# Performance work log

Hardware: AMD Instinct MI355X
Metric: run time of the kernel (lower is better)

## Reference

```python
import jax, jax.numpy as jnp
import numpy as np

B, L, D = 2, 2048, 1024
H = 16
DH = D // H
FACTOR = 0.6
U = max(1, min(L, int(FACTOR * L)))  # 1228 selected queries


def setup_inputs() -> dict:
    key = jax.random.key(0)
    ks = jax.random.split(key, 9)
    s = 0.02
    return {
        "x": jax.random.normal(ks[0], (B, L, D), dtype=jnp.float32),
        "Wq": jax.random.normal(ks[1], (D, D), dtype=jnp.float32) * s,
        "bq": jnp.zeros((D,), dtype=jnp.float32),
        "Wk": jax.random.normal(ks[2], (D, D), dtype=jnp.float32) * s,
        "bk": jnp.zeros((D,), dtype=jnp.float32),
        "Wv": jax.random.normal(ks[3], (D, D), dtype=jnp.float32) * s,
        "bv": jnp.zeros((D,), dtype=jnp.float32),
        "Wo": jax.random.normal(ks[4], (D, D), dtype=jnp.float32) * s,
        "bo": jnp.zeros((D,), dtype=jnp.float32),
    }


def _split_heads(x):
    b, l, d = x.shape
    return x.reshape(b, l, H, DH).transpose(0, 2, 1, 3)  # [b,h,l,dh]


def reference(x, Wq, bq, Wk, bk, Wv, bv, Wo, bo):
    b, l, _ = x.shape
    scale = 1.0 / jnp.sqrt(jnp.asarray(DH, dtype=x.dtype))

    q = _split_heads(x @ Wq + bq)  # [b,h,l,dh]
    k = _split_heads(x @ Wk + bk)
    v = _split_heads(x @ Wv + bv)

    # full scores for sparsity heuristic
    scores = jnp.einsum("bhqd,bhkd->bhqk", q, k) * scale  # [b,h,l,l]
    sparsity = scores.max(axis=-1) - scores.mean(axis=-1)  # [b,h,l]

    _, top_idx = jax.lax.top_k(sparsity, U)  # [b,h,U]

    # gather selected queries, attend only on those rows
    q_sel = jnp.take_along_axis(q, top_idx[..., None], axis=2)  # [b,h,U,dh]
    scores_sel = jnp.einsum("bhud,bhkd->bhuk", q_sel, k) * scale  # [b,h,U,l]
    attn = jax.nn.softmax(scores_sel, axis=-1)
    out_sel = jnp.einsum("bhuk,bhkd->bhud", attn, v)  # [b,h,U,dh]

    # scatter back into zero-initialized output
    bi = jnp.arange(b)[:, None, None]
    hi = jnp.arange(H)[None, :, None]
    out = jnp.zeros_like(q).at[bi, hi, top_idx].set(out_sel)  # [b,h,l,dh]

    out = out.transpose(0, 2, 1, 3).reshape(b, l, D)
    return out @ Wo + bo
```

## Files before the change

### kernel.cpp

```cpp
#include <hip/hip_runtime.h>
#include <math.h>
#include <stdint.h>

#define Bn 2
#define Ln 2048
#define Dn 1024
#define Hn 16
#define DHn 64
#define Un 1228
#define BHn (Bn*Hn)
#define SCALE 0.125f
#define WIN 32
#define WHALF 16
#define SXf 16.0f
#define SWf 256.0f
#define SQf 16.0f
#define SVf 16.0f
#define SPf 16.0f
#define ESC_PROJ (1.0f / 4096.0f)
#define ESC_OUT  (1.0f / 65536.0f)
#define PSC (SCALE / 256.0f)
#define QPS 88

typedef _Float16 f16;
typedef __attribute__((ext_vector_type(8))) _Float16 f16x8;
typedef __attribute__((ext_vector_type(4))) float f32x4;
struct h4s { f16 x, y, z, w; };

__device__ __forceinline__ void splitf16(float f, f16& hi, f16& lo) {
  hi = (f16)f;
  lo = (f16)(f - (float)hi);
}

__device__ __forceinline__ void gl_lds16(const void* g, void* l) {
  __builtin_amdgcn_global_load_lds(
      (const __attribute__((address_space(1))) void*)g,
      (__attribute__((address_space(3))) void*)l, 16, 0, 0);
}

#define MFMA(a, b, c) __builtin_amdgcn_mfma_f32_16x16x32_f16((a), (b), (c), 0, 0, 0)

__global__ __launch_bounds__(256) void split_kernel(
    const float* __restrict__ in, f16* __restrict__ oh, f16* __restrict__ ol, int n4) {
  int i = blockIdx.x * 256 + threadIdx.x;
  if (i >= n4) return;
  float4 v = ((const float4*)in)[i];
  h4s h, l;
  splitf16(v.x * SXf, h.x, l.x); splitf16(v.y * SXf, h.y, l.y);
  splitf16(v.z * SXf, h.z, l.z); splitf16(v.w * SXf, h.w, l.w);
  ((h4s*)oh)[i] = h; ((h4s*)ol)[i] = l;
}

__global__ __launch_bounds__(256) void tsplit_w4(
    const float* __restrict__ W0, const float* __restrict__ W1,
    const float* __restrict__ W2, const float* __restrict__ W3,
    f16* __restrict__ oh, f16* __restrict__ ol) {
  __shared__ float ts[64][65];
  const int t = threadIdx.x;
  const int r0 = blockIdx.x * 64, c0 = blockIdx.y * 64;
  const int z = blockIdx.z;
  const float* in = (z == 0) ? W0 : (z == 1) ? W1 : (z == 2) ? W2 : W3;
#pragma unroll
  for (int c = 0; c < 4; ++c) {
    int f = (c * 256 + t) * 4; int row = f >> 6, col = f & 63;
    float4 v = *(const float4*)&in[(size_t)(r0 + row) * Dn + c0 + col];
    ts[row][col] = v.x; ts[row][col + 1] = v.y; ts[row][col + 2] = v.z; ts[row][col + 3] = v.w;
  }
  __syncthreads();
#pragma unroll
  for (int c = 0; c < 4; ++c) {
    int f = (c * 256 + t) * 4; int crow = f >> 6, rcol = f & 63;
    h4s h, l;
    splitf16(ts[rcol + 0][crow] * SWf, h.x, l.x);
    splitf16(ts[rcol + 1][crow] * SWf, h.y, l.y);
    splitf16(ts[rcol + 2][crow] * SWf, h.z, l.z);
    splitf16(ts[rcol + 3][crow] * SWf, h.w, l.w);
    size_t o = (size_t)(z * 1024 + c0 + crow) * Dn + r0 + rcol;
    *(h4s*)&oh[o] = h; *(h4s*)&ol[o] = l;
  }
}

__global__ void gemm_qkv(
    const f16* __restrict__ Ah, const f16* __restrict__ Al,
    const f16* __restrict__ Bth, const f16* __restrict__ Btl,
    const float* __restrict__ bq, const float* __restrict__ bk, const float* __restrict__ bv,
    float* __restrict__ Qf, f16* __restrict__ Qbh,
    float* __restrict__ Kf, f16* __restrict__ Kbh,
    f16* __restrict__ Vh16, int K) {
  __shared__ f16 sAh[128 * 32], sAl[128 * 32], sBh[128 * 32], sBl[128 * 32];
  const int t = threadIdx.x;
  const int w = t >> 6, lane = t & 63, lm = lane & 15, q = lane >> 4;
  const int wr = w >> 1, wc = w & 1;
  const int n0 = blockIdx.x * 128, m0 = blockIdx.y * 128;
  f32x4 acc[4][4] = {};
  for (int k0 = 0; k0 < K; k0 += 32) {
    const f16* s0 = Ah + (size_t)m0 * K + k0;
    const f16* s1 = Al + (size_t)m0 * K + k0;
    const f16* s2 = Bth + (size_t)n0 * K + k0;
    const f16* s3 = Btl + (size_t)n0 * K + k0;
#pragma unroll
    for (int c = 0; c < 2; ++c) {
      int f = (c * 256 + t) * 8; int row = f >> 5, col = f & 31;
      size_t go = (size_t)row * K + col;
      gl_lds16(s0 + go, &sAh[f]);
      gl_lds16(s1 + go, &sAl[f]);
      gl_lds16(s2 + go, &sBh[f]);
      gl_lds16(s3 + go, &sBl[f]);
    }
    __syncthreads();
    f16x8 a_h[4], a_l[4], b_h[4], b_l[4];
#pragma unroll
    for (int mi = 0; mi < 4; ++mi) {
      int r = (wr * 64 + mi * 16 + lm) * 32 + q * 8;
      a_h[mi] = *(const f16x8*)&sAh[r];
      a_l[mi] = *(const f16x8*)&sAl[r];
    }
#pragma unroll
    for (int ni = 0; ni < 4; ++ni) {
      int r = (wc * 64 + ni * 16 + lm) * 32 + q * 8;
      b_h[ni] = *(const f16x8*)&sBh[r];
      b_l[ni] = *(const f16x8*)&sBl[r];
    }
#pragma unroll
    for (int mi = 0; mi < 4; ++mi)
#pragma unroll
      for (int ni = 0; ni < 4; ++ni) {
        acc[mi][ni] = MFMA(a_h[mi], b_h[ni], acc[mi][ni]);
        acc[mi][ni] = MFMA(a_h[mi], b_l[ni], acc[mi][ni]);
        acc[mi][ni] = MFMA(a_l[mi], b_h[ni], acc[mi][ni]);
      }
    __syncthreads();
  }
#pragma unroll
  for (int mi = 0; mi < 4; ++mi)
#pragma unroll
    for (int ni = 0; ni < 4; ++ni) {
      int nglob = n0 + wc * 64 + ni * 16;
      int seg = nglob >> 10;
      int c = (nglob & 1023) + lm;
      const float* bp = (seg == 0) ? bq : (seg == 1) ? bk : bv;
      float bvv = bp[c];
#pragma unroll
      for (int r = 0; r < 4; ++r) {
        int grow = m0 + wr * 64 + mi * 16 + q * 4 + r;
        float v = acc[mi][ni][r] * ESC_PROJ + bvv;
        size_t o = (size_t)grow * 1024 + c;
        if (seg == 0) {
          Qf[o] = v;
          Qbh[o] = (f16)(v * SQf);
        } else if (seg == 1) {
          Kf[o] = v;
          Kbh[o] = (f16)(v * SQf);
        } else {
          Vh16[o] = (f16)(v * SVf);
        }
      }
    }
}

__global__ __launch_bounds__(256) void tsplit_v(
    const f16* __restrict__ Vh16, f16* __restrict__ out) {
  __shared__ f16 ts[64][72];
  const int t = threadIdx.x;
  const int l0 = blockIdx.x * 64;
  const int bh = blockIdx.y, b = bh >> 4, h = bh & 15;
#pragma unroll
  for (int c = 0; c < 2; ++c) {
    int e = c * 256 + t; int row = e >> 3, cg = e & 7;
    *(uint4*)&ts[row][cg * 8] =
        *(const uint4*)&Vh16[((size_t)b * Ln + l0 + row) * Dn + h * DHn + cg * 8];
  }
  __syncthreads();
#pragma unroll
  for (int c = 0; c < 2; ++c) {
    int e = c * 256 + t; int drow = e >> 3, lg = e & 7;
    f16 tmp[8];
#pragma unroll
    for (int j = 0; j < 8; ++j) tmp[j] = ts[lg * 8 + j][drow];
    *(uint4*)&out[((size_t)bh * DHn + drow) * Ln + l0 + lg * 8] = *(uint4*)tmp;
  }
}

__global__ __launch_bounds__(256, 4) void gemm_a1(
    const f16* __restrict__ A,
    const f16* __restrict__ Bth, const f16* __restrict__ Btl,
    const float* __restrict__ bias, float escale,
    float* __restrict__ Cf, int M, int N, int K) {
  __shared__ f16 sA[128 * 32], sBh[64 * 32], sBl[64 * 32];
  const int t = threadIdx.x;
  const int w = t >> 6, lane = t & 63, lm = lane & 15, q = lane >> 4;
  const int wr = w >> 1, wc = w & 1;
  const int n0 = blockIdx.x * 64, m0 = blockIdx.y * 128;
  f32x4 acc[4][2] = {};
  for (int k0 = 0; k0 < K; k0 += 32) {
    const f16* s0 = A + (size_t)m0 * K + k0;
    const f16* s2 = Bth + (size_t)n0 * K + k0;
    const f16* s3 = Btl + (size_t)n0 * K + k0;
#pragma unroll
    for (int c = 0; c < 2; ++c) {
      int f = (c * 256 + t) * 8; int row = f >> 5, col = f & 31;
      gl_lds16(s0 + (size_t)row * K + col, &sA[f]);
    }
    {
      int f = t * 8; int row = f >> 5, col = f & 31;
      gl_lds16(s2 + (size_t)row * K + col, &sBh[f]);
      gl_lds16(s3 + (size_t)row * K + col, &sBl[f]);
    }
    __syncthreads();
    f16x8 a_[4], b_h[2], b_l[2];
#pragma unroll
    for (int mi = 0; mi < 4; ++mi)
      a_[mi] = *(const f16x8*)&sA[(wr * 64 + mi * 16 + lm) * 32 + q * 8];
#pragma unroll
    for (int ni = 0; ni < 2; ++ni) {
      int r = (wc * 32 + ni * 16 + lm) * 32 + q * 8;
      b_h[ni] = *(const f16x8*)&sBh[r];
      b_l[ni] = *(const f16x8*)&sBl[r];
    }
#pragma unroll
    for (int mi = 0; mi < 4; ++mi)
#pragma unroll
      for (int ni = 0; ni < 2; ++ni) {
        acc[mi][ni] = MFMA(a_[mi], b_h[ni], acc[mi][ni]);
        acc[mi][ni] = MFMA(a_[mi], b_l[ni], acc[mi][ni]);
      }
    __syncthreads();
  }
#pragma unroll
  for (int mi = 0; mi < 4; ++mi)
#pragma unroll
    for (int ni = 0; ni < 2; ++ni) {
      int gcol = n0 + wc * 32 + ni * 16 + lm;
      float bvv = bias[gcol];
#pragma unroll
      for (int r = 0; r < 4; ++r) {
        int grow = m0 + wr * 64 + mi * 16 + q * 4 + r;
        Cf[(size_t)grow * N + gcol] = acc[mi][ni][r] * escale + bvv;
      }
    }
}

__global__ __launch_bounds__(256) void ksum_part(
    const f16* __restrict__ Kh, float* __restrict__ ksum) {
  __shared__ float red[4][64];
  const int t = threadIdx.x, d = t & 63, seg = t >> 6;
  const int bx = blockIdx.x, bh = blockIdx.y, b = bh >> 4, h = bh & 15;
  float s = 0.f;
  const int lbase = bx * 256 + seg * 64;
  for (int r = 0; r < 64; ++r) {
    size_t o = ((size_t)b * Ln + lbase + r) * Dn + h * DHn + d;
    s += (float)Kh[o];
  }
  red[seg][d] = s;
  __syncthreads();
  if (t < 64) atomicAdd(&ksum[bh * DHn + t], red[0][t] + red[1][t] + red[2][t] + red[3][t]);
}

__global__ __launch_bounds__(256, 2) void attn_stats_mfma(
    const f16* __restrict__ Qh, const f16* __restrict__ Kh,
    const float* __restrict__ ksum,
    float* __restrict__ row_max, float* __restrict__ spars) {
  __shared__ f16 sQh[128 * 64], sKh[128 * 64];
  __shared__ float redm[128][5];
  const int t = threadIdx.x;
  const int w = t >> 6, lane = t & 63, lm = lane & 15, q = lane >> 4;
  const int bh = blockIdx.y, b = bh >> 4, h = bh & 15;
  const int q0 = blockIdx.x * 128;
  const f16* qsh = Qh + ((size_t)b * Ln + q0) * Dn + h * DHn;
#pragma unroll
  for (int c = 0; c < 4; ++c) {
    int f = (c * 256 + t) * 8; int row = f >> 6, c16 = (f >> 3) & 7;
    size_t go = (size_t)row * Dn + ((c16 ^ (row & 7)) << 3);
    gl_lds16(qsh + go, &sQh[f]);
  }
  __syncthreads();
  f16x8 a_h[8][2];
#pragma unroll
  for (int mi = 0; mi < 8; ++mi)
#pragma unroll
    for (int ks = 0; ks < 2; ++ks) {
      int row = mi * 16 + lm;
      int r = row * 64 + (((ks * 4 + q) ^ (row & 7)) << 3);
      a_h[mi][ks] = *(const f16x8*)&sQh[r];
    }
  float rmax[8][4];
#pragma unroll
  for (int mi = 0; mi < 8; ++mi)
#pragma unroll
    for (int r = 0; r < 4; ++r) rmax[mi][r] = -1e30f;

  for (int kt = 0; kt < Ln / 128; ++kt) {
    __syncthreads();
    const f16* ksh = Kh + ((size_t)b * Ln + kt * 128) * Dn + h * DHn;
#pragma unroll
    for (int c = 0; c < 4; ++c) {
      int f = (c * 256 + t) * 8; int row = f >> 6, c16 = (f >> 3) & 7;
      size_t go = (size_t)row * Dn + ((c16 ^ (row & 7)) << 3);
      gl_lds16(ksh + go, &sKh[f]);
    }
    __syncthreads();
#pragma unroll
    for (int ni = 0; ni < 2; ++ni) {
      int bcol = (w * 2 + ni) * 16;
      f16x8 b_h[2];
#pragma unroll
      for (int ks = 0; ks < 2; ++ks) {
        int row = bcol + lm;
        int r = row * 64 + (((ks * 4 + q) ^ (row & 7)) << 3);
        b_h[ks] = *(const f16x8*)&sKh[r];
      }
#pragma unroll
      for (int mi = 0; mi < 8; ++mi) {
        f32x4 acc = {0.f, 0.f, 0.f, 0.f};
        __builtin_amdgcn_s_setprio(1);
        acc = MFMA(a_h[mi][0], b_h[0], acc);
        acc = MFMA(a_h[mi][1], b_h[1], acc);
        __builtin_amdgcn_s_setprio(0);
#pragma unroll
        for (int r = 0; r < 4; ++r) rmax[mi][r] = fmaxf(rmax[mi][r], acc[r]);
      }
    }
  }
#pragma unroll
  for (int mi = 0; mi < 8; ++mi)
#pragma unroll
    for (int r = 0; r < 4; ++r) {
      float v = rmax[mi][r];
      v = fmaxf(v, __shfl_xor(v, 1)); v = fmaxf(v, __shfl_xor(v, 2));
      v = fmaxf(v, __shfl_xor(v, 4)); v = fmaxf(v, __shfl_xor(v, 8));
      if (lm == 0) redm[mi * 16 + q * 4 + r][w] = v;
    }
  __syncthreads();
  if (t < 128) {
    float m = fmaxf(fmaxf(redm[t][0], redm[t][1]), fmaxf(redm[t][2], redm[t][3]));
    float dot = 0.f;
    const float* kp = ksum + bh * DHn;
#pragma unroll
    for (int d = 0; d < 64; ++d) {
      int idx = t * 64 + ((((d >> 3) ^ (t & 7)) << 3) | (d & 7));
      dot += (float)sQh[idx] * kp[d];
    }
    row_max[(size_t)bh * Ln + q0 + t] = m * PSC;
    spars[(size_t)bh * Ln + q0 + t] = m * PSC - dot * (PSC / (float)Ln);
  }
}

__global__ __launch_bounds__(1024) void topk_sort(
    const float* __restrict__ spars, int* __restrict__ top_idx, int* __restrict__ wrow) {
  __shared__ unsigned long long keys[Ln];
  const int t = threadIdx.x;
  const int bh = blockIdx.x;
  for (int i = t; i < Ln; i += 1024) {
    unsigned u = __float_as_uint(spars[(size_t)bh * Ln + i]);
    u = (u & 0x80000000u) ? ~u : (u | 0x80000000u);
    u = ~u;
    keys[i] = ((unsigned long long)u << 32) | (unsigned)i;
  }
  __syncthreads();
  for (int k = 2; k <= Ln; k <<= 1) {
    for (int j = k >> 1; j > 0; j >>= 1) {
      int i = ((t & ~(j - 1)) << 1) | (t & (j - 1));
      int ixj = i | j;
      unsigned long long a = keys[i], bb = keys[ixj];
      bool up = ((i & k) == 0);
      if ((a > bb) == up) { keys[i] = bb; keys[ixj] = a; }
      __syncthreads();
    }
  }
  for (int u = t; u < Un - WHALF; u += 1024)
    top_idx[(size_t)bh * Un + u] = (int)(keys[u] & 0xFFFFFFFFu);
  if (t < WIN) wrow[bh * WIN + t] = (int)(keys[Un - WHALF + t] & 0xFFFFFFFFu);
}

__global__ __launch_bounds__(256) void refine_rows(
    const float* __restrict__ Qf, const float* __restrict__ Kf,
    const int* __restrict__ wrow, float* __restrict__ spx) {
  __shared__ float qs[64];
  __shared__ float redm[4], reds[4];
  const int t = threadIdx.x;
  const int j = blockIdx.x, bh = blockIdx.y, b = bh >> 4, h = bh & 15;
  const int qi = wrow[bh * WIN + j];
  if (t < 64) qs[t] = Qf[((size_t)b * Ln + qi) * Dn + h * DHn + t];
  __syncthreads();
  float mx = -1e30f, sm = 0.f;
  for (int ki = t; ki < Ln; ki += 256) {
    const float* kp = &Kf[((size_t)b * Ln + ki) * Dn + h * DHn];
    float s = 0.f;
#pragma unroll
    for (int d0 = 0; d0 < 64; d0 += 4) {
      float4 k4 = *(const float4*)&kp[d0];
      s = fmaf(k4.x, qs[d0], s);
      s = fmaf(k4.y, qs[d0 + 1], s);
      s = fmaf(k4.z, qs[d0 + 2], s);
      s = fmaf(k4.w, qs[d0 + 3], s);
    }
    mx = fmaxf(mx, s); sm += s;
  }
  const int w = t >> 6, lane = t & 63;
#pragma unroll
  for (int off = 1; off < 64; off <<= 1) {
    mx = fmaxf(mx, __shfl_xor(mx, off));
    sm += __shfl_xor(sm, off);
  }
  if (lane == 0) { redm[w] = mx; reds[w] = sm; }
  __syncthreads();
  if (t == 0) {
    float m = fmaxf(fmaxf(redm[0], redm[1]), fmaxf(redm[2], redm[3]));
    float s = reds[0] + reds[1] + reds[2] + reds[3];
    spx[bh * WIN + j] = SCALE * (m - s * (1.0f / (float)Ln));
  }
}

__global__ __launch_bounds__(64) void topk_final(
    const float* __restrict__ spx, const int* __restrict__ wrow,
    int* __restrict__ top_idx) {
  const int bh = blockIdx.x;
  if (threadIdx.x != 0) return;
  float v[WIN]; int r[WIN];
#pragma unroll
  for (int j = 0; j < WIN; ++j) { v[j] = spx[bh * WIN + j]; r[j] = wrow[bh * WIN + j]; }
  unsigned taken = 0;
  for (int s = 0; s < WHALF; ++s) {
    int best = -1;
    for (int j = 0; j < WIN; ++j) {
      if (taken & (1u << j)) continue;
      if (best < 0 || v[j] > v[best] || (v[j] == v[best] && r[j] < r[best])) best = j;
    }
    taken |= 1u << best;
    top_idx[(size_t)bh * Un + (Un - WHALF) + s] = r[best];
  }
}

__global__ __launch_bounds__(256, 4) void attn_sel_part(
    const f16* __restrict__ Qh, const f16* __restrict__ Kh,
    const f16* __restrict__ Vth,
    const int* __restrict__ topi, const float* __restrict__ row_max,
    float* __restrict__ pO, float* __restrict__ pD) {
  __shared__ f16 sK[64 * 64], sV[64 * 64];
  __shared__ f16 sQP[64 * QPS];
  __shared__ float rmL[64];
  __shared__ int qxL[64];
  __shared__ float dred[64][5];
  const int t = threadIdx.x;
  const int w = t >> 6, lane = t & 63, lm = lane & 15, q = lane >> 4;
  const int half = blockIdx.y & 1, bh = blockIdx.y >> 1, b = bh >> 4, h = bh & 15;
  const int u0 = blockIdx.x * 64;
  const int nrows = (Un - u0 < 64) ? (Un - u0) : 64;
  if (t < 64) {
    int qi = topi[(size_t)bh * Un + ((t < nrows) ? (u0 + t) : 0)];
    qxL[t] = qi;
    rmL[t] = row_max[(size_t)bh * Ln + qi];
  }
  __syncthreads();
#pragma unroll
  for (int c = 0; c < 2; ++c) {
    int f = (c * 256 + t) * 8; int row = f >> 6, col = f & 63;
    size_t go = ((size_t)b * Ln + qxL[row]) * Dn + h * DHn + col;
    *(uint4*)&sQP[row * QPS + col] = *(const uint4*)&Qh[go];
  }
  __syncthreads();
  f16x8 aq[4][2];
#pragma unroll
  for (int mi = 0; mi < 4; ++mi)
#pragma unroll
    for (int ks = 0; ks < 2; ++ks)
      aq[mi][ks] = *(const f16x8*)&sQP[(mi * 16 + lm) * QPS + ks * 32 + q * 8];
  f32x4 oacc[4] = {};
  float dacc[4][4] = {};

  const f16* kbase = Kh + (size_t)b * Ln * Dn + h * DHn;
  const f16* vbase = Vth + (size_t)bh * DHn * Ln;
  for (int kt = 0; kt < 16; ++kt) {
    const int l0 = half * 1024 + kt * 64;
    __syncthreads();
#pragma unroll
    for (int c = 0; c < 2; ++c) {
      int f = (c * 256 + t) * 8; int row = f >> 6, c16 = (f >> 3) & 7;
      int sc = (c16 ^ (row & 7)) << 3;
      gl_lds16(kbase + (size_t)(l0 + row) * Dn + sc, &sK[f]);
      gl_lds16(vbase + (size_t)row * Ln + l0 + sc, &sV[f]);
    }
    __syncthreads();
    f16x8 kb[2];
#pragma unroll
    for (int ks = 0; ks < 2; ++ks) {
      int row = w * 16 + lm;
      kb[ks] = *(const f16x8*)&sK[row * 64 + (((ks * 4 + q) ^ (row & 7)) << 3)];
    }
#pragma unroll
    for (int mi = 0; mi < 4; ++mi) {
      f32x4 acc = {0.f, 0.f, 0.f, 0.f};
      __builtin_amdgcn_s_setprio(1);
      acc = MFMA(aq[mi][0], kb[0], acc);
      acc = MFMA(aq[mi][1], kb[1], acc);
      __builtin_amdgcn_s_setprio(0);
#pragma unroll
      for (int r = 0; r < 4; ++r) {
        int row = mi * 16 + q * 4 + r;
        float p = __expf(acc[r] * PSC - rmL[row]);
        dacc[mi][r] += p;
        sQP[row * QPS + w * 16 + lm] = (f16)(p * SPf);
      }
    }
    __syncthreads();
    f16x8 vb[2];
#pragma unroll
    for (int ks = 0; ks < 2; ++ks) {
      int row = w * 16 + lm;
      vb[ks] = *(const f16x8*)&sV[row * 64 + (((ks * 4 + q) ^ (row & 7)) << 3)];
    }
#pragma unroll
    for (int mi = 0; mi < 4; ++mi) {
      f16x8 pf0 = *(const f16x8*)&sQP[(mi * 16 + lm) * QPS + 0 * 32 + q * 8];
      f16x8 pf1 = *(const f16x8*)&sQP[(mi * 16 + lm) * QPS + 1 * 32 + q * 8];
      __builtin_amdgcn_s_setprio(1);
      oacc[mi] = MFMA(pf0, vb[0], oacc[mi]);
      oacc[mi] = MFMA(pf1, vb[1], oacc[mi]);
      __builtin_amdgcn_s_setprio(0);
    }
  }
#pragma unroll
  for (int mi = 0; mi < 4; ++mi)
#pragma unroll
    for (int r = 0; r < 4; ++r) {
      float v = dacc[mi][r];
      v += __shfl_xor(v, 1); v += __shfl_xor(v, 2);
      v += __shfl_xor(v, 4); v += __shfl_xor(v, 8);
      if (lm == 0) dred[mi * 16 + q * 4 + r][w] = v;
    }
  __syncthreads();
  const size_t pbase = ((size_t)half * BHn + bh) * 1280 + u0;
  if (t < 64)
    pD[pbase + t] = dred[t][0] + dred[t][1] + dred[t][2] + dred[t][3];
#pragma unroll
  for (int mi = 0; mi < 4; ++mi)
#pragma unroll
    for (int r = 0; r < 4; ++r) {
      int row = mi * 16 + q * 4 + r;
      pO[(pbase + row) * 64 + w * 16 + lm] = oacc[mi][r];
    }
}

__global__ __launch_bounds__(256) void attn_combine(
    const float* __restrict__ pO, const float* __restrict__ pD,
    const int* __restrict__ topi, f16* __restrict__ AOh) {
  const int t = threadIdx.x;
  const int u0 = blockIdx.x * 64, bh = blockIdx.y, b = bh >> 4, h = bh & 15;
  const int nrows = (Un - u0 < 64) ? (Un - u0) : 64;
  const int row = t >> 2, pg = t & 3;
  if (row >= nrows) return;
  int qi = topi[(size_t)bh * Un + u0 + row];
  size_t i0 = (size_t)bh * 1280 + u0 + row;
  size_t i1 = (size_t)BHn * 1280 + i0;
  float dinv = 1.0f / (pD[i0] + pD[i1]);
  const float* p0 = &pO[i0 * 64 + pg * 16];
  const float* p1 = &pO[i1 * 64 + pg * 16];
  f16 buf[16];
#pragma unroll
  for (int c = 0; c < 4; ++c) {
    float4 a = *(const float4*)&p0[c * 4];
    float4 bb = *(const float4*)&p1[c * 4];
    buf[c * 4 + 0] = (f16)((a.x + bb.x) * dinv);
    buf[c * 4 + 1] = (f16)((a.y + bb.y) * dinv);
    buf[c * 4 + 2] = (f16)((a.z + bb.z) * dinv);
    buf[c * 4 + 3] = (f16)((a.w + bb.w) * dinv);
  }
  f16* dst = &AOh[((size_t)b * Ln + qi) * Dn + h * DHn + pg * 16];
  *(uint4*)&dst[0] = *(uint4*)&buf[0];
  *(uint4*)&dst[8] = *(uint4*)&buf[8];
}

extern "C" void kernel_launch(void* const* d_in, const int* in_sizes, int n_in,
                              void* d_out, int out_size, void* d_ws, size_t ws_size,
                              hipStream_t stream) {
  (void)in_sizes; (void)n_in; (void)out_size; (void)ws_size;
  const float* x  = (const float*)d_in[0];
  const float* Wq = (const float*)d_in[1];
  const float* bq = (const float*)d_in[2];
  const float* Wk = (const float*)d_in[3];
  const float* bk = (const float*)d_in[4];
  const float* Wv = (const float*)d_in[5];
  const float* bv = (const float*)d_in[6];
  const float* Wo = (const float*)d_in[7];
  const float* bo = (const float*)d_in[8];
  float* out = (float*)d_out;

  uint8_t* p = (uint8_t*)d_ws;
  const size_t NE = (size_t)Bn * Ln * Dn;
  f16* xh = (f16*)p;  p += NE * 2;
  f16* xl = (f16*)p;  p += NE * 2;
  f16* Wt_h = (f16*)p; p += (size_t)4096 * Dn * 2;
  f16* Wt_l = (f16*)p; p += (size_t)4096 * Dn * 2;
  f16* Qbh = (f16*)p; p += NE * 2;
  f16* Qbl = (f16*)p; p += NE * 2;
  f16* Kbh = (f16*)p; p += NE * 2;
  f16* Kbl = (f16*)p; p += NE * 2;
  float* Qf = (float*)p;  p += NE * 4;
  float* Kf = (float*)p;  p += NE * 4;
  f16* Vh16 = (f16*)p; p += NE * 2;
  f16* Vth  = (f16*)p; p += NE * 2;
  float* rowmax = (float*)p; p += (size_t)BHn * Ln * 4;
  float* spars  = (float*)p; p += (size_t)BHn * Ln * 4;
  float* ksum   = (float*)p; p += (size_t)BHn * DHn * 4;
  int* topi     = (int*)p;   p += (size_t)BHn * Un * 4;
  int* wrow     = (int*)p;   p += (size_t)BHn * WIN * 4;
  float* spx    = (float*)p; p += (size_t)BHn * WIN * 4;
  float* pD     = (float*)p; p += (size_t)2 * BHn * 1280 * 4;
  float* pO = Qf;
  f16* AOh = xh;
  (void)Qbl; (void)Kbl;

  dim3 blk(256);
  hipLaunchKernelGGL(split_kernel, dim3((int)(NE / 4 / 256)), blk, 0, stream, x, xh, xl, (int)(NE / 4));
  hipLaunchKernelGGL(tsplit_w4, dim3(16, 16, 4), blk, 0, stream, Wq, Wk, Wv, Wo, Wt_h, Wt_l);
  hipLaunchKernelGGL(gemm_qkv, dim3(24, 32), blk, 0, stream, xh, xl, Wt_h, Wt_l,
                     bq, bk, bv, Qf, Qbh, Kf, Kbh, Vh16, Dn);
  hipLaunchKernelGGL(tsplit_v, dim3(Ln / 64, BHn), blk, 0, stream, Vh16, Vth);
  hipMemsetAsync(ksum, 0, (size_t)BHn * DHn * 4, stream);
  hipLaunchKernelGGL(ksum_part, dim3(8, BHn), blk, 0, stream, Kbh, ksum);
  hipLaunchKernelGGL(attn_stats_mfma, dim3(Ln / 128, BHn), blk, 0, stream,
                     Qbh, Kbh, ksum, rowmax, spars);
  hipLaunchKernelGGL(topk_sort, dim3(BHn), dim3(1024), 0, stream, spars, topi, wrow);
  hipLaunchKernelGGL(refine_rows, dim3(WIN, BHn), blk, 0, stream, Qf, Kf, wrow, spx);
  hipLaunchKernelGGL(topk_final, dim3(BHn), dim3(64), 0, stream, spx, wrow, topi);
  hipMemsetAsync(AOh, 0, NE * 2, stream);
  hipLaunchKernelGGL(attn_sel_part, dim3((Un + 63) / 64, 2 * BHn), blk, 0, stream,
                     Qbh, Kbh, Vth, topi, rowmax, pO, pD);
  hipLaunchKernelGGL(attn_combine, dim3((Un + 63) / 64, BHn), blk, 0, stream,
                     pO, pD, topi, AOh);
  hipLaunchKernelGGL(gemm_a1, dim3(16, 32), blk, 0, stream, AOh,
                     Wt_h + (size_t)3072 * Dn, Wt_l + (size_t)3072 * Dn, bo,
                     ESC_OUT, out, Bn * Ln, Dn, Dn);
}
```

Before: 456.1 us.

## Batch all boundary-window rows per K tile in fp32 refinement

```diff
diff --git a/kernel.cpp b/kernel.cpp
--- a/kernel.cpp
+++ b/kernel.cpp
@@ -372,62 +372,90 @@
   if (t < WIN) wrow[bh * WIN + t] = (int)(keys[Un - WHALF + t] & 0xFFFFFFFFu);
 }
 
-__global__ __launch_bounds__(256) void refine_rows(
+__global__ __launch_bounds__(256) void refine_part(
     const float* __restrict__ Qf, const float* __restrict__ Kf,
-    const int* __restrict__ wrow, float* __restrict__ spx) {
-  __shared__ float qs[64];
-  __shared__ float redm[4], reds[4];
-  const int t = threadIdx.x;
-  const int j = blockIdx.x, bh = blockIdx.y, b = bh >> 4, h = bh & 15;
-  const int qi = wrow[bh * WIN + j];
-  if (t < 64) qs[t] = Qf[((size_t)b * Ln + qi) * Dn + h * DHn + t];
-  __syncthreads();
-  float mx = -1e30f, sm = 0.f;
-  for (int ki = t; ki < Ln; ki += 256) {
-    const float* kp = &Kf[((size_t)b * Ln + ki) * Dn + h * DHn];
-    float s = 0.f;
-#pragma unroll
-    for (int d0 = 0; d0 < 64; d0 += 4) {
-      float4 k4 = *(const float4*)&kp[d0];
-      s = fmaf(k4.x, qs[d0], s);
-      s = fmaf(k4.y, qs[d0 + 1], s);
-      s = fmaf(k4.z, qs[d0 + 2], s);
-      s = fmaf(k4.w, qs[d0 + 3], s);
-    }
-    mx = fmaxf(mx, s); sm += s;
+    const int* __restrict__ wrow,
+    float* __restrict__ pmaxf, float* __restrict__ psum) {
+  __shared__ float qs[WIN][68];
+  __shared__ float redm[4][WIN], reds[4][WIN];
+  const int t = threadIdx.x;
+  const int bx = blockIdx.x, bh = blockIdx.y, b = bh >> 4, h = bh & 15;
+  {
+    int j = t >> 3, d0 = (t & 7) * 8;
+    int qi = wrow[bh * WIN + j];
+    const float* qp = &Qf[((size_t)b * Ln + qi) * Dn + h * DHn + d0];
+    *(float4*)&qs[j][d0] = *(const float4*)qp;
+    *(float4*)&qs[j][d0 + 4] = *(const float4*)(qp + 4);
+  }
+  __syncthreads();
+  const int ki = bx * 256 + t;
+  const float* kp = &Kf[((size_t)b * Ln + ki) * Dn + h * DHn];
+  float s[WIN];
+#pragma unroll
+  for (int j = 0; j < WIN; ++j) s[j] = 0.f;
+#pragma unroll 4
+  for (int d0 = 0; d0 < 64; d0 += 4) {
+    float4 k4 = *(const float4*)&kp[d0];
+#pragma unroll
+    for (int j = 0; j < WIN; ++j) {
+      float4 q4 = *(const float4*)&qs[j][d0];
+      s[j] = fmaf(k4.x, q4.x, s[j]);
+      s[j] = fmaf(k4.y, q4.y, s[j]);
+      s[j] = fmaf(k4.z, q4.z, s[j]);
+      s[j] = fmaf(k4.w, q4.w, s[j]);
+    }
   }
   const int w = t >> 6, lane = t & 63;
 #pragma unroll
-  for (int off = 1; off < 64; off <<= 1) {
-    mx = fmaxf(mx, __shfl_xor(mx, off));
-    sm += __shfl_xor(sm, off);
-  }
-  if (lane == 0) { redm[w] = mx; reds[w] = sm; }
-  __syncthreads();
-  if (t == 0) {
-    float m = fmaxf(fmaxf(redm[0], redm[1]), fmaxf(redm[2], redm[3]));
-    float s = reds[0] + reds[1] + reds[2] + reds[3];
-    spx[bh * WIN + j] = SCALE * (m - s * (1.0f / (float)Ln));
+  for (int j = 0; j < WIN; ++j) {
+    float mx = s[j], sm = s[j];
+#pragma unroll
+    for (int off = 1; off < 64; off <<= 1) {
+      mx = fmaxf(mx, __shfl_xor(mx, off));
+      sm += __shfl_xor(sm, off);
+    }
+    if (lane == 0) { redm[w][j] = mx; reds[w][j] = sm; }
+  }
+  __syncthreads();
+  if (t < WIN) {
+    float mx = fmaxf(fmaxf(redm[0][t], redm[1][t]), fmaxf(redm[2][t], redm[3][t]));
+    float sm = reds[0][t] + reds[1][t] + reds[2][t] + reds[3][t];
+    size_t o = ((size_t)bh * WIN + t) * 8 + bx;
+    pmaxf[o] = mx;
+    psum[o] = sm;
   }
 }
 
 __global__ __launch_bounds__(64) void topk_final(
-    const float* __restrict__ spx, const int* __restrict__ wrow,
-    int* __restrict__ top_idx) {
+    const float* __restrict__ pmaxf, const float* __restrict__ psum,
+    const int* __restrict__ wrow, int* __restrict__ top_idx) {
+  __shared__ float spxL[WIN];
   const int bh = blockIdx.x;
-  if (threadIdx.x != 0) return;
+  const int t = threadIdx.x;
+  if (t < WIN) {
+    float m = -1e30f, s = 0.f;
+#pragma unroll
+    for (int p = 0; p < 8; ++p) {
+      size_t o = ((size_t)bh * WIN + t) * 8 + p;
+      m = fmaxf(m, pmaxf[o]);
+      s += psum[o];
+    }
+    spxL[t] = SCALE * (m - s * (1.0f / (float)Ln));
+  }
+  __syncthreads();
+  if (t != 0) return;
   float v[WIN]; int r[WIN];
 #pragma unroll
-  for (int j = 0; j < WIN; ++j) { v[j] = spx[bh * WIN + j]; r[j] = wrow[bh * WIN + j]; }
+  for (int j = 0; j < WIN; ++j) { v[j] = spxL[j]; r[j] = wrow[bh * WIN + j]; }
   unsigned taken = 0;
-  for (int s = 0; s < WHALF; ++s) {
+  for (int s2 = 0; s2 < WHALF; ++s2) {
     int best = -1;
     for (int j = 0; j < WIN; ++j) {
       if (taken & (1u << j)) continue;
       if (best < 0 || v[j] > v[best] || (v[j] == v[best] && r[j] < r[best])) best = j;
     }
     taken |= 1u << best;
-    top_idx[(size_t)bh * Un + (Un - WHALF) + s] = r[best];
+    top_idx[(size_t)bh * Un + (Un - WHALF) + s2] = r[best];
   }
 }
 
@@ -592,9 +620,7 @@
   f16* Wt_h = (f16*)p; p += (size_t)4096 * Dn * 2;
   f16* Wt_l = (f16*)p; p += (size_t)4096 * Dn * 2;
   f16* Qbh = (f16*)p; p += NE * 2;
-  f16* Qbl = (f16*)p; p += NE * 2;
   f16* Kbh = (f16*)p; p += NE * 2;
-  f16* Kbl = (f16*)p; p += NE * 2;
   float* Qf = (float*)p;  p += NE * 4;
   float* Kf = (float*)p;  p += NE * 4;
   f16* Vh16 = (f16*)p; p += NE * 2;
@@ -604,11 +630,11 @@
   float* ksum   = (float*)p; p += (size_t)BHn * DHn * 4;
   int* topi     = (int*)p;   p += (size_t)BHn * Un * 4;
   int* wrow     = (int*)p;   p += (size_t)BHn * WIN * 4;
-  float* spx    = (float*)p; p += (size_t)BHn * WIN * 4;
+  float* pmaxf  = (float*)p; p += (size_t)BHn * WIN * 8 * 4;
+  float* psum   = (float*)p; p += (size_t)BHn * WIN * 8 * 4;
   float* pD     = (float*)p; p += (size_t)2 * BHn * 1280 * 4;
   float* pO = Qf;
   f16* AOh = xh;
-  (void)Qbl; (void)Kbl;
 
   dim3 blk(256);
   hipLaunchKernelGGL(split_kernel, dim3((int)(NE / 4 / 256)), blk, 0, stream, x, xh, xl, (int)(NE / 4));
@@ -621,8 +647,8 @@
   hipLaunchKernelGGL(attn_stats_mfma, dim3(Ln / 128, BHn), blk, 0, stream,
                      Qbh, Kbh, ksum, rowmax, spars);
   hipLaunchKernelGGL(topk_sort, dim3(BHn), dim3(1024), 0, stream, spars, topi, wrow);
-  hipLaunchKernelGGL(refine_rows, dim3(WIN, BHn), blk, 0, stream, Qf, Kf, wrow, spx);
-  hipLaunchKernelGGL(topk_final, dim3(BHn), dim3(64), 0, stream, spx, wrow, topi);
+  hipLaunchKernelGGL(refine_part, dim3(8, BHn), blk, 0, stream, Qf, Kf, wrow, pmaxf, psum);
+  hipLaunchKernelGGL(topk_final, dim3(BHn), dim3(64), 0, stream, pmaxf, psum, wrow, topi);
   hipMemsetAsync(AOh, 0, NE * 2, stream);
   hipLaunchKernelGGL(attn_sel_part, dim3((Un + 63) / 64, 2 * BHn), blk, 0, stream,
                      Qbh, Kbh, Vth, topi, rowmax, pO, pD);
```

After: 384.0 us. 1.19x faster.
